# Kernel optimization log

Measured on AMD Instinct MI355X. Metric: run time of the kernel, lower is better.

## Reference

```python
import jax, jax.numpy as jnp
import numpy as np

B, S, H, DH = 1, 4096, 8, 40  # hardcoded in the original forward
D = H * DH  # 320

def setup_inputs() -> dict:
    key = jax.random.key(0)
    ks = jax.random.split(key, 6)
    s = 1.0 / np.sqrt(D)
    return {
        "x": jax.random.normal(ks[0], (B, S, D), dtype=jnp.float32),
        "Wq": jax.random.normal(ks[1], (D, D), dtype=jnp.float32) * s,
        "Wk": jax.random.normal(ks[2], (D, D), dtype=jnp.float32) * s,
        "Wv": jax.random.normal(ks[3], (D, D), dtype=jnp.float32) * s,
        "Wo": jax.random.normal(ks[4], (D, D), dtype=jnp.float32) * s,
        "bo": jnp.zeros((D,), dtype=jnp.float32),
    }

def reference(x, Wq, Wk, Wv, Wo, bo):
    scale = DH ** (-0.5)
    # nn.Linear(bias=False): y = x @ W^T. context = x (self-attention).
    q = x @ Wq.T
    k = x @ Wk.T
    v = x @ Wv.T
    # split heads: [B,S,D] -> [B*H, S, DH]
    def split_heads(t):
        return t.reshape(B, S, H, DH).transpose(0, 2, 1, 3).reshape(B * H, S, DH)
    q, k, v = split_heads(q), split_heads(k), split_heads(v)
    # fp32 QK^T (original forces float), softmax, AV
    sim = jnp.einsum('bid,bjd->bij', q.astype(jnp.float32), k.astype(jnp.float32)) * scale
    attn = jax.nn.softmax(sim, axis=-1)
    out = jnp.einsum('bij,bjd->bid', attn, v)
    # merge heads: [B*H, S, DH] -> [B, S, D]
    out = out.reshape(B, H, S, DH).transpose(0, 2, 1, 3).reshape(B, S, D)
    return out @ Wo.T + bo
```

## Files before the change

kernel.cpp:

```cpp
#include <hip/hip_runtime.h>
#include <math.h>


#define NS 4096
#define ND 320
#define SCALE2 0.2281101152f
#define HS48 196608
#define VTH 163840
#define XN 1310720

typedef __attribute__((ext_vector_type(8))) short bf16x8;
typedef __attribute__((ext_vector_type(16))) float f32x16;

static __device__ __forceinline__ unsigned short f2bru(float f) {
  return (unsigned short)((__builtin_bit_cast(unsigned int, f) + 0x8000u) >> 16);
}
static __device__ __forceinline__ unsigned int pk2ru(float a, float b) {
  unsigned int ua = __builtin_bit_cast(unsigned int, a) + 0x8000u;
  unsigned int ub = __builtin_bit_cast(unsigned int, b) + 0x8000u;
  return __builtin_amdgcn_perm(ub, ua, 0x07060302u);
}
static __device__ __forceinline__ unsigned int pk2t(float a, float b) {
  return __builtin_amdgcn_perm(__builtin_bit_cast(unsigned int, b),
                               __builtin_bit_cast(unsigned int, a), 0x07060302u);
}
static __device__ __forceinline__ float fexp2(float x) {
  return __builtin_amdgcn_exp2f(x);
}
static __device__ __forceinline__ bf16x8 ld8(const unsigned short* p) {
  union { uint2 u[2]; bf16x8 v; } c;
  c.u[0] = *(const uint2*)p;
  c.u[1] = *(const uint2*)(p + 4);
  return c.v;
}
static __device__ __forceinline__ uint4 ld16u(const unsigned short* p) {
  uint2 a = *(const uint2*)p, b = *(const uint2*)(p + 4);
  return make_uint4(a.x, a.y, b.x, b.y);
}
static __device__ __forceinline__ void st16(unsigned short* p, uint4 v) {
  *(uint2*)p = make_uint2(v.x, v.y);
  *(uint2*)(p + 4) = make_uint2(v.z, v.w);
}
static __device__ __forceinline__ int sig32(int q) {
  int s = q >> 4, h2 = (q >> 3) & 1, j = q & 7;
  return (s << 4) | ((j >> 2) << 3) | (h2 << 2) | (j & 3);
}

__global__ __launch_bounds__(256) void proj_qkv_kernel(
    const float* __restrict__ x, const float* __restrict__ Wq,
    const float* __restrict__ Wk, const float* __restrict__ Wv,
    unsigned short* __restrict__ Qp, unsigned short* __restrict__ Kp,
    unsigned short* __restrict__ Vt) {
  const int z = blockIdx.z;
  const float* W = (z == 0) ? Wq : (z == 1) ? Wk : Wv;
  __shared__ __align__(16) unsigned short As[64 * 36];
  __shared__ __align__(16) unsigned short Bs[64 * 36];
  __shared__ __align__(16) unsigned short Tile[64 * 76];
  const int t = threadIdx.x;
  const int w = t >> 6, l = t & 63, l31 = l & 31, hi = l >> 5;
  const int bm = blockIdx.x * 64, bn = blockIdx.y * 64;
  const int m0 = (w & 1) * 32, n0 = (w >> 1) * 32;
  f32x16 acc = {0,0,0,0,0,0,0,0,0,0,0,0,0,0,0,0};
  const int ar = t >> 2, ac = t & 3;
  const float* gA = x + (bm + ar) * ND + ac * 8;
  const float* gB = W + (bn + ar) * ND + ac * 8;
  unsigned short* lA = As + ar * 36 + ac * 8;
  unsigned short* lB = Bs + ar * 36 + ac * 8;
  const unsigned short* af = As + (m0 + l31) * 36 + hi * 8;
  const unsigned short* bf = Bs + (n0 + l31) * 36 + hi * 8;
  float4 a0 = *(const float4*)gA, a1 = *(const float4*)(gA + 4);
  float4 b0 = *(const float4*)gB, b1 = *(const float4*)(gB + 4);
  for (int k0 = 0; k0 < ND; k0 += 32) {
    __syncthreads();
    st16(lA, make_uint4(pk2ru(a0.x, a0.y), pk2ru(a0.z, a0.w),
                        pk2ru(a1.x, a1.y), pk2ru(a1.z, a1.w)));
    st16(lB, make_uint4(pk2ru(b0.x, b0.y), pk2ru(b0.z, b0.w),
                        pk2ru(b1.x, b1.y), pk2ru(b1.z, b1.w)));
    __syncthreads();
    if (k0 + 32 < ND) {
      gA += 32; gB += 32;
      a0 = *(const float4*)gA; a1 = *(const float4*)(gA + 4);
      b0 = *(const float4*)gB; b1 = *(const float4*)(gB + 4);
    }
    bf16x8 A0 = ld8(af), A1 = ld8(af + 16);
    bf16x8 B0 = ld8(bf), B1 = ld8(bf + 16);
    acc = __builtin_amdgcn_mfma_f32_32x32x16_bf16(A0, B0, acc, 0, 0, 0);
    acc = __builtin_amdgcn_mfma_f32_32x32x16_bf16(A1, B1, acc, 0, 0, 0);
  }
  if (z < 2) {
    unsigned short* Y = (z == 0) ? Qp : Kp;
    const float sc = (z == 0) ? SCALE2 : 1.0f;
    const unsigned int padw = (z == 0) ? 0xC200u : 0x3F80u;
#pragma unroll
    for (int r2 = 0; r2 < 16; r2++) {
      int lr = m0 + (r2 & 3) + 8 * (r2 >> 2) + 4 * hi;
      Tile[lr * 68 + n0 + l31] = f2bru(acc[r2] * sc);
    }
    __syncthreads();
    for (int i = t; i < 512; i += 256) {
      int row = i >> 3, ch = i & 7;
      int j = bn + ch * 8;
      int h = j / 40, dh = j - h * 40;
      uint4 v = ld16u(Tile + row * 68 + ch * 8);
      unsigned short* dst = Y + h * HS48 + (bm + row) * 48 + dh;
      st16(dst, v);
      if (dh == 0)
        st16(Y + h * HS48 + (bm + row) * 48 + 40, make_uint4(padw, 0u, 0u, 0u));
    }
  } else {
#pragma unroll
    for (int r2 = 0; r2 < 16; r2++) {
      int lr = m0 + (r2 & 3) + 8 * (r2 >> 2) + 4 * hi;
      Tile[(n0 + l31) * 76 + lr] = f2bru(acc[r2]);
    }
    __syncthreads();
    for (int i = t; i < 512; i += 256) {
      int row = i >> 3, ch = i & 7;
      int j = bn + row;
      int h = j / 40, dd = j - h * 40;
      uint4 v = ld16u(Tile + row * 76 + ch * 8);
      st16(Vt + h * VTH + dd * NS + bm + ch * 8, v);
    }
  }
}

__global__ __launch_bounds__(256) void attn_kernel(
    const unsigned short* __restrict__ Qp, const unsigned short* __restrict__ Kp,
    const unsigned short* __restrict__ Vt, unsigned short* __restrict__ Op,
    float* __restrict__ Lp) {
  const int b = blockIdx.x;
  const int h = b & 7, ks = (b >> 3) & 7, qt = b >> 6;
  const int t = threadIdx.x;
  const int w = t >> 6, l = t & 63, l31 = l & 31, hi = l >> 5;
  __shared__ __align__(16) unsigned short Ks[64 * 68];
  __shared__ __align__(16) unsigned short Vs[48 * 68];
  for (int i = t; i < 272; i += 256)
    ((unsigned int*)(Vs + 40 * 68))[i] = (i < 34) ? 0x3F803F80u : 0u;

  const int kbase = ks * 512;
  const int qbase = qt * 128 + w * 32;
  const unsigned short* qp = Qp + h * HS48 + (qbase + l31) * 48 + hi * 8;
  bf16x8 qf0 = *(const bf16x8*)qp;
  bf16x8 qf1 = *(const bf16x8*)(qp + 16);
  bf16x8 qf2 = *(const bf16x8*)(qp + 32);

  f32x16 oa0 = {0,0,0,0,0,0,0,0,0,0,0,0,0,0,0,0};
  f32x16 oa1 = {0,0,0,0,0,0,0,0,0,0,0,0,0,0,0,0};

  const int kr0 = t / 6, kc0 = t - kr0 * 6;
  const int kr1 = (t + 256) / 6, kc1 = (t + 256) - kr1 * 6;
  const unsigned short* gK0 = Kp + h * HS48 + (kbase + kr0) * 48 + kc0 * 8;
  const unsigned short* gK1 = Kp + h * HS48 + (kbase + kr1) * 48 + kc1 * 8;
  unsigned short* lK0 = Ks + ((kr0 & 32) | sig32(kr0 & 31)) * 68 + kc0 * 8;
  unsigned short* lK1 = Ks + ((kr1 & 32) | sig32(kr1 & 31)) * 68 + kc1 * 8;
  const int vr0 = t >> 3, vc = t & 7, vr1 = 32 + vr0;
  const unsigned short* gV0 = Vt + h * VTH + vr0 * NS + kbase + vc * 8;
  const unsigned short* gV1 = Vt + h * VTH + vr1 * NS + kbase + vc * 8;
  unsigned short* lV0 = Vs + vr0 * 68 + vc * 8;
  unsigned short* lV1 = Vs + vr1 * 68 + vc * 8;

  const unsigned short* kf0 = Ks + l31 * 68 + hi * 8;
  const unsigned short* kf1 = Ks + (32 + l31) * 68 + hi * 8;
  const unsigned short* vf0 = Vs + l31 * 68 + hi * 8;
  const unsigned short* vf1 = Vs + (32 + (l31 & 15)) * 68 + hi * 8;

  uint4 ka = *(const uint4*)gK0;
  uint4 kb2, vb2;
  uint4 va = *(const uint4*)gV0;
  if (t < 128) kb2 = *(const uint4*)gK1;
  if (t < 64)  vb2 = *(const uint4*)gV1;

  for (int it = 0; it < 8; ++it) {
    __syncthreads();
    st16(lK0, ka);
    if (t < 128) st16(lK1, kb2);
    st16(lV0, va);
    if (t < 64) st16(lV1, vb2);
    __syncthreads();
    gK0 += 64 * 48; gK1 += 64 * 48; gV0 += 64; gV1 += 64;
    ka = *(const uint4*)gK0;
    va = *(const uint4*)gV0;
    if (t < 128) kb2 = *(const uint4*)gK1;
    if (t < 64)  vb2 = *(const uint4*)gV1;

    unsigned int pw0[8], pw1[8];
    {
      f32x16 s0 = {0,0,0,0,0,0,0,0,0,0,0,0,0,0,0,0};
      s0 = __builtin_amdgcn_mfma_f32_32x32x16_bf16(ld8(kf0), qf0, s0, 0, 0, 0);
      s0 = __builtin_amdgcn_mfma_f32_32x32x16_bf16(ld8(kf0 + 16), qf1, s0, 0, 0, 0);
      s0 = __builtin_amdgcn_mfma_f32_32x32x16_bf16(ld8(kf0 + 32), qf2, s0, 0, 0, 0);
#pragma unroll
      for (int i = 0; i < 8; i++)
        pw0[i] = pk2t(fexp2(s0[2 * i]), fexp2(s0[2 * i + 1]));
    }
    {
      f32x16 s1 = {0,0,0,0,0,0,0,0,0,0,0,0,0,0,0,0};
      s1 = __builtin_amdgcn_mfma_f32_32x32x16_bf16(ld8(kf1), qf0, s1, 0, 0, 0);
      s1 = __builtin_amdgcn_mfma_f32_32x32x16_bf16(ld8(kf1 + 16), qf1, s1, 0, 0, 0);
      s1 = __builtin_amdgcn_mfma_f32_32x32x16_bf16(ld8(kf1 + 32), qf2, s1, 0, 0, 0);
#pragma unroll
      for (int i = 0; i < 8; i++)
        pw1[i] = pk2t(fexp2(s1[2 * i]), fexp2(s1[2 * i + 1]));
    }
    bf16x8 pf0 = __builtin_bit_cast(bf16x8, make_uint4(pw0[0], pw0[1], pw0[2], pw0[3]));
    bf16x8 pf1 = __builtin_bit_cast(bf16x8, make_uint4(pw0[4], pw0[5], pw0[6], pw0[7]));
    bf16x8 pf2 = __builtin_bit_cast(bf16x8, make_uint4(pw1[0], pw1[1], pw1[2], pw1[3]));
    bf16x8 pf3 = __builtin_bit_cast(bf16x8, make_uint4(pw1[4], pw1[5], pw1[6], pw1[7]));
    oa0 = __builtin_amdgcn_mfma_f32_32x32x16_bf16(pf0, ld8(vf0), oa0, 0, 0, 0);
    oa1 = __builtin_amdgcn_mfma_f32_32x32x16_bf16(pf0, ld8(vf1), oa1, 0, 0, 0);
    oa0 = __builtin_amdgcn_mfma_f32_32x32x16_bf16(pf1, ld8(vf0 + 16), oa0, 0, 0, 0);
    oa1 = __builtin_amdgcn_mfma_f32_32x32x16_bf16(pf1, ld8(vf1 + 16), oa1, 0, 0, 0);
    oa0 = __builtin_amdgcn_mfma_f32_32x32x16_bf16(pf2, ld8(vf0 + 32), oa0, 0, 0, 0);
    oa1 = __builtin_amdgcn_mfma_f32_32x32x16_bf16(pf2, ld8(vf1 + 32), oa1, 0, 0, 0);
    oa0 = __builtin_amdgcn_mfma_f32_32x32x16_bf16(pf3, ld8(vf0 + 48), oa0, 0, 0, 0);
    oa1 = __builtin_amdgcn_mfma_f32_32x32x16_bf16(pf3, ld8(vf1 + 48), oa1, 0, 0, 0);
  }

  unsigned short* opb = Op + ks * XN + h * 163840;
  float* lpb = Lp + ks * 32768 + h * NS;
#pragma unroll
  for (int r2 = 0; r2 < 16; r2++) {
    int qr = qbase + (r2 & 3) + 8 * (r2 >> 2) + 4 * hi;
    opb[qr * 40 + l31] = f2bru(oa0[r2]);
    if (l31 < 8) opb[qr * 40 + 32 + l31] = f2bru(oa1[r2]);
    if (l31 == 8) lpb[qr] = oa1[r2];
  }
}

__global__ __launch_bounds__(256) void proj_out_kernel(
    const unsigned short* __restrict__ Op, const float* __restrict__ Lp,
    const float* __restrict__ Wo, const float* __restrict__ bo,
    float* __restrict__ out) {
  __shared__ __align__(16) unsigned short As[64 * 36];
  __shared__ __align__(16) unsigned short Bs[64 * 36];
  __shared__ float invL[512];
  const int t = threadIdx.x;
  const int w = t >> 6, l = t & 63, l31 = l & 31, hi = l >> 5;
  const int bm = blockIdx.x * 64, bn = blockIdx.y * 64;
  const int m0 = (w & 1) * 32, n0 = (w >> 1) * 32;
  f32x16 acc = {0,0,0,0,0,0,0,0,0,0,0,0,0,0,0,0};
  const int ar = t >> 2, ac = t & 3;

  for (int i = t; i < 512; i += 256) {
    int h2 = i >> 6, sl = i & 63;
    float ls = 0.f;
#pragma unroll
    for (int k = 0; k < 8; k++) ls += Lp[k * 32768 + h2 * NS + bm + sl];
    invL[i] = 1.0f / ls;
  }

  const float* gB = Wo + (bn + ar) * ND + ac * 8;
  unsigned short* lA = As + ar * 36 + ac * 8;
  unsigned short* lB = Bs + ar * 36 + ac * 8;
  const unsigned short* af = As + (m0 + l31) * 36 + hi * 8;
  const unsigned short* bf = Bs + (n0 + l31) * 36 + hi * 8;

  int d0 = ac * 8;
  int h2 = d0 / 40, dh = d0 - h2 * 40;
  const unsigned short* opb = Op + h2 * 163840 + (bm + ar) * 40 + dh;
  uint4 u[8];
#pragma unroll
  for (int k = 0; k < 8; k++) u[k] = *(const uint4*)(opb + k * XN);
  float4 b0 = *(const float4*)gB, b1 = *(const float4*)(gB + 4);

  for (int k0 = 0; k0 < ND; k0 += 32) {
    __syncthreads();
    {
      float a0 = 0.f, a1 = 0.f, a2 = 0.f, a3 = 0.f;
      float a4 = 0.f, a5 = 0.f, a6 = 0.f, a7 = 0.f;
#pragma unroll
      for (int k = 0; k < 8; k++) {
        a0 += __builtin_bit_cast(float, u[k].x << 16);
        a1 += __builtin_bit_cast(float, u[k].x & 0xFFFF0000u);
        a2 += __builtin_bit_cast(float, u[k].y << 16);
        a3 += __builtin_bit_cast(float, u[k].y & 0xFFFF0000u);
        a4 += __builtin_bit_cast(float, u[k].z << 16);
        a5 += __builtin_bit_cast(float, u[k].z & 0xFFFF0000u);
        a6 += __builtin_bit_cast(float, u[k].w << 16);
        a7 += __builtin_bit_cast(float, u[k].w & 0xFFFF0000u);
      }
      float inv = invL[h2 * 64 + ar];
      st16(lA, make_uint4(pk2ru(a0 * inv, a1 * inv), pk2ru(a2 * inv, a3 * inv),
                          pk2ru(a4 * inv, a5 * inv), pk2ru(a6 * inv, a7 * inv)));
    }
    st16(lB, make_uint4(pk2ru(b0.x, b0.y), pk2ru(b0.z, b0.w),
                        pk2ru(b1.x, b1.y), pk2ru(b1.z, b1.w)));
    __syncthreads();
    if (k0 + 32 < ND) {
      d0 += 32;
      h2 = d0 / 40; dh = d0 - h2 * 40;
      opb = Op + h2 * 163840 + (bm + ar) * 40 + dh;
#pragma unroll
      for (int k = 0; k < 8; k++) u[k] = *(const uint4*)(opb + k * XN);
      gB += 32;
      b0 = *(const float4*)gB; b1 = *(const float4*)(gB + 4);
    }
    bf16x8 A0 = ld8(af), A1 = ld8(af + 16);
    bf16x8 B0 = ld8(bf), B1 = ld8(bf + 16);
    acc = __builtin_amdgcn_mfma_f32_32x32x16_bf16(A0, B0, acc, 0, 0, 0);
    acc = __builtin_amdgcn_mfma_f32_32x32x16_bf16(A1, B1, acc, 0, 0, 0);
  }
  const int j = bn + n0 + l31;
  const float bj = bo[j];
#pragma unroll
  for (int r2 = 0; r2 < 16; r2++) {
    int row = bm + m0 + (r2 & 3) + 8 * (r2 >> 2) + 4 * hi;
    out[row * ND + j] = acc[r2] + bj;
  }
}

extern "C" void kernel_launch(void* const* d_in, const int* in_sizes, int n_in,
                              void* d_out, int out_size, void* d_ws, size_t ws_size,
                              hipStream_t stream) {
  (void)in_sizes; (void)n_in; (void)out_size; (void)ws_size;
  const float* x  = (const float*)d_in[0];
  const float* Wq = (const float*)d_in[1];
  const float* Wk = (const float*)d_in[2];
  const float* Wv = (const float*)d_in[3];
  const float* Wo = (const float*)d_in[4];
  const float* bo = (const float*)d_in[5];
  float* out = (float*)d_out;

  unsigned short* Qp = (unsigned short*)d_ws;
  unsigned short* Kp = Qp + 8 * HS48;
  unsigned short* Vt = Kp + 8 * HS48;
  unsigned short* Op = Vt + 8 * VTH;
  float* Lp = (float*)(Op + 8 * XN);

  proj_qkv_kernel<<<dim3(64, 5, 3), 256, 0, stream>>>(x, Wq, Wk, Wv, Qp, Kp, Vt);
  attn_kernel<<<dim3(2048), 256, 0, stream>>>(Qp, Kp, Vt, Op, Lp);
  proj_out_kernel<<<dim3(64, 5), 256, 0, stream>>>(Op, Lp, Wo, bo, out);
}
```

Measured before the change: 135.4 us.

## Retile projections to 128x64 with K=64 and split combine into separate kernel

The QKV and output projection GEMMs move to 128x64 block tiles that step K by 64 and keep two accumulators per wave, which raises MFMA work per barrier and reuses each A fragment. The split-K attention partials are now reduced and normalized by a new combine kernel that writes a bf16 merged-head activation, so the output projection just loads it. The attention inner loop also interleaves the PV MFMAs with each score block to shorten live ranges. The cost is one extra kernel launch and an extra global round trip of the combined activation, and fewer blocks in the GEMMs, which lowers occupancy.

```diff
diff --git a/kernel.cpp b/kernel.cpp
--- a/kernel.cpp
+++ b/kernel.cpp
@@ -51,74 +51,91 @@
     const float* __restrict__ Wk, const float* __restrict__ Wv,
     unsigned short* __restrict__ Qp, unsigned short* __restrict__ Kp,
     unsigned short* __restrict__ Vt) {
-  const int z = blockIdx.z;
+  const int zi = blockIdx.y;
+  const int z = zi / 5;
+  const int bnn = (zi - z * 5) * 64;
   const float* W = (z == 0) ? Wq : (z == 1) ? Wk : Wv;
-  __shared__ __align__(16) unsigned short As[64 * 36];
-  __shared__ __align__(16) unsigned short Bs[64 * 36];
-  __shared__ __align__(16) unsigned short Tile[64 * 76];
+  __shared__ __align__(16) unsigned short As[128 * 76];
+  __shared__ __align__(16) unsigned short Bs[64 * 76];
   const int t = threadIdx.x;
   const int w = t >> 6, l = t & 63, l31 = l & 31, hi = l >> 5;
-  const int bm = blockIdx.x * 64, bn = blockIdx.y * 64;
-  const int m0 = (w & 1) * 32, n0 = (w >> 1) * 32;
-  f32x16 acc = {0,0,0,0,0,0,0,0,0,0,0,0,0,0,0,0};
-  const int ar = t >> 2, ac = t & 3;
-  const float* gA = x + (bm + ar) * ND + ac * 8;
-  const float* gB = W + (bn + ar) * ND + ac * 8;
-  unsigned short* lA = As + ar * 36 + ac * 8;
-  unsigned short* lB = Bs + ar * 36 + ac * 8;
-  const unsigned short* af = As + (m0 + l31) * 36 + hi * 8;
-  const unsigned short* bf = Bs + (n0 + l31) * 36 + hi * 8;
-  float4 a0 = *(const float4*)gA, a1 = *(const float4*)(gA + 4);
-  float4 b0 = *(const float4*)gB, b1 = *(const float4*)(gB + 4);
-  for (int k0 = 0; k0 < ND; k0 += 32) {
-    __syncthreads();
-    st16(lA, make_uint4(pk2ru(a0.x, a0.y), pk2ru(a0.z, a0.w),
-                        pk2ru(a1.x, a1.y), pk2ru(a1.z, a1.w)));
-    st16(lB, make_uint4(pk2ru(b0.x, b0.y), pk2ru(b0.z, b0.w),
-                        pk2ru(b1.x, b1.y), pk2ru(b1.z, b1.w)));
-    __syncthreads();
-    if (k0 + 32 < ND) {
-      gA += 32; gB += 32;
-      a0 = *(const float4*)gA; a1 = *(const float4*)(gA + 4);
-      b0 = *(const float4*)gB; b1 = *(const float4*)(gB + 4);
-    }
-    bf16x8 A0 = ld8(af), A1 = ld8(af + 16);
-    bf16x8 B0 = ld8(bf), B1 = ld8(bf + 16);
-    acc = __builtin_amdgcn_mfma_f32_32x32x16_bf16(A0, B0, acc, 0, 0, 0);
-    acc = __builtin_amdgcn_mfma_f32_32x32x16_bf16(A1, B1, acc, 0, 0, 0);
-  }
+  const int bm = blockIdx.x * 128;
+  const int m0 = w * 32;
+  f32x16 acc0 = {0,0,0,0,0,0,0,0,0,0,0,0,0,0,0,0};
+  f32x16 acc1 = {0,0,0,0,0,0,0,0,0,0,0,0,0,0,0,0};
+  const unsigned short* af = As + (m0 + l31) * 76 + hi * 8;
+  const unsigned short* bf0 = Bs + l31 * 76 + hi * 8;
+  const unsigned short* bf1 = Bs + (32 + l31) * 76 + hi * 8;
+  for (int k0 = 0; k0 < ND; k0 += 64) {
+    __syncthreads();
+#pragma unroll
+    for (int i = 0; i < 4; i++) {
+      int c = t + i * 256;
+      int row = c >> 3, kc = (c & 7) << 3;
+      const float* g = x + (bm + row) * ND + k0 + kc;
+      float4 v0 = *(const float4*)g, v1 = *(const float4*)(g + 4);
+      st16(As + row * 76 + kc,
+           make_uint4(pk2ru(v0.x, v0.y), pk2ru(v0.z, v0.w),
+                      pk2ru(v1.x, v1.y), pk2ru(v1.z, v1.w)));
+    }
+#pragma unroll
+    for (int i = 0; i < 2; i++) {
+      int c = t + i * 256;
+      int row = c >> 3, kc = (c & 7) << 3;
+      const float* g = W + (bnn + row) * ND + k0 + kc;
+      float4 v0 = *(const float4*)g, v1 = *(const float4*)(g + 4);
+      st16(Bs + row * 76 + kc,
+           make_uint4(pk2ru(v0.x, v0.y), pk2ru(v0.z, v0.w),
+                      pk2ru(v1.x, v1.y), pk2ru(v1.z, v1.w)));
+    }
+    __syncthreads();
+#pragma unroll
+    for (int ks = 0; ks < 4; ks++) {
+      bf16x8 A = ld8(af + ks * 16);
+      acc0 = __builtin_amdgcn_mfma_f32_32x32x16_bf16(A, ld8(bf0 + ks * 16), acc0, 0, 0, 0);
+      acc1 = __builtin_amdgcn_mfma_f32_32x32x16_bf16(A, ld8(bf1 + ks * 16), acc1, 0, 0, 0);
+    }
+  }
+  __syncthreads();
   if (z < 2) {
+    unsigned short* Tile = As;
     unsigned short* Y = (z == 0) ? Qp : Kp;
     const float sc = (z == 0) ? SCALE2 : 1.0f;
     const unsigned int padw = (z == 0) ? 0xC200u : 0x3F80u;
 #pragma unroll
     for (int r2 = 0; r2 < 16; r2++) {
       int lr = m0 + (r2 & 3) + 8 * (r2 >> 2) + 4 * hi;
-      Tile[lr * 68 + n0 + l31] = f2bru(acc[r2] * sc);
-    }
-    __syncthreads();
-    for (int i = t; i < 512; i += 256) {
-      int row = i >> 3, ch = i & 7;
-      int j = bn + ch * 8;
+      Tile[lr * 68 + l31] = f2bru(acc0[r2] * sc);
+      Tile[lr * 68 + 32 + l31] = f2bru(acc1[r2] * sc);
+    }
+    __syncthreads();
+#pragma unroll
+    for (int i = 0; i < 4; i++) {
+      int c = t + i * 256;
+      int row = c >> 3, ch = c & 7;
+      int j = bnn + ch * 8;
       int h = j / 40, dh = j - h * 40;
       uint4 v = ld16u(Tile + row * 68 + ch * 8);
-      unsigned short* dst = Y + h * HS48 + (bm + row) * 48 + dh;
-      st16(dst, v);
+      st16(Y + h * HS48 + (bm + row) * 48 + dh, v);
       if (dh == 0)
         st16(Y + h * HS48 + (bm + row) * 48 + 40, make_uint4(padw, 0u, 0u, 0u));
     }
   } else {
+    unsigned short* Tile = As;
 #pragma unroll
     for (int r2 = 0; r2 < 16; r2++) {
       int lr = m0 + (r2 & 3) + 8 * (r2 >> 2) + 4 * hi;
-      Tile[(n0 + l31) * 76 + lr] = f2bru(acc[r2]);
-    }
-    __syncthreads();
-    for (int i = t; i < 512; i += 256) {
-      int row = i >> 3, ch = i & 7;
-      int j = bn + row;
+      Tile[l31 * 132 + lr] = f2bru(acc0[r2]);
+      Tile[(32 + l31) * 132 + lr] = f2bru(acc1[r2]);
+    }
+    __syncthreads();
+#pragma unroll
+    for (int i = 0; i < 4; i++) {
+      int c = t + i * 256;
+      int row = c >> 4, ch = c & 15;
+      int j = bnn + row;
       int h = j / 40, dd = j - h * 40;
-      uint4 v = ld16u(Tile + row * 76 + ch * 8);
+      uint4 v = ld16u(Tile + row * 132 + ch * 8);
       st16(Vt + h * VTH + dd * NS + bm + ch * 8, v);
     }
   }
@@ -183,37 +200,38 @@
     if (t < 128) kb2 = *(const uint4*)gK1;
     if (t < 64)  vb2 = *(const uint4*)gV1;
 
-    unsigned int pw0[8], pw1[8];
     {
       f32x16 s0 = {0,0,0,0,0,0,0,0,0,0,0,0,0,0,0,0};
       s0 = __builtin_amdgcn_mfma_f32_32x32x16_bf16(ld8(kf0), qf0, s0, 0, 0, 0);
       s0 = __builtin_amdgcn_mfma_f32_32x32x16_bf16(ld8(kf0 + 16), qf1, s0, 0, 0, 0);
       s0 = __builtin_amdgcn_mfma_f32_32x32x16_bf16(ld8(kf0 + 32), qf2, s0, 0, 0, 0);
+      unsigned int pw[8];
 #pragma unroll
       for (int i = 0; i < 8; i++)
-        pw0[i] = pk2t(fexp2(s0[2 * i]), fexp2(s0[2 * i + 1]));
+        pw[i] = pk2t(fexp2(s0[2 * i]), fexp2(s0[2 * i + 1]));
+      bf16x8 pf0 = __builtin_bit_cast(bf16x8, make_uint4(pw[0], pw[1], pw[2], pw[3]));
+      bf16x8 pf1 = __builtin_bit_cast(bf16x8, make_uint4(pw[4], pw[5], pw[6], pw[7]));
+      oa0 = __builtin_amdgcn_mfma_f32_32x32x16_bf16(pf0, ld8(vf0), oa0, 0, 0, 0);
+      oa1 = __builtin_amdgcn_mfma_f32_32x32x16_bf16(pf0, ld8(vf1), oa1, 0, 0, 0);
+      oa0 = __builtin_amdgcn_mfma_f32_32x32x16_bf16(pf1, ld8(vf0 + 16), oa0, 0, 0, 0);
+      oa1 = __builtin_amdgcn_mfma_f32_32x32x16_bf16(pf1, ld8(vf1 + 16), oa1, 0, 0, 0);
     }
     {
       f32x16 s1 = {0,0,0,0,0,0,0,0,0,0,0,0,0,0,0,0};
       s1 = __builtin_amdgcn_mfma_f32_32x32x16_bf16(ld8(kf1), qf0, s1, 0, 0, 0);
       s1 = __builtin_amdgcn_mfma_f32_32x32x16_bf16(ld8(kf1 + 16), qf1, s1, 0, 0, 0);
       s1 = __builtin_amdgcn_mfma_f32_32x32x16_bf16(ld8(kf1 + 32), qf2, s1, 0, 0, 0);
+      unsigned int pw[8];
 #pragma unroll
       for (int i = 0; i < 8; i++)
-        pw1[i] = pk2t(fexp2(s1[2 * i]), fexp2(s1[2 * i + 1]));
-    }
-    bf16x8 pf0 = __builtin_bit_cast(bf16x8, make_uint4(pw0[0], pw0[1], pw0[2], pw0[3]));
-    bf16x8 pf1 = __builtin_bit_cast(bf16x8, make_uint4(pw0[4], pw0[5], pw0[6], pw0[7]));
-    bf16x8 pf2 = __builtin_bit_cast(bf16x8, make_uint4(pw1[0], pw1[1], pw1[2], pw1[3]));
-    bf16x8 pf3 = __builtin_bit_cast(bf16x8, make_uint4(pw1[4], pw1[5], pw1[6], pw1[7]));
-    oa0 = __builtin_amdgcn_mfma_f32_32x32x16_bf16(pf0, ld8(vf0), oa0, 0, 0, 0);
-    oa1 = __builtin_amdgcn_mfma_f32_32x32x16_bf16(pf0, ld8(vf1), oa1, 0, 0, 0);
-    oa0 = __builtin_amdgcn_mfma_f32_32x32x16_bf16(pf1, ld8(vf0 + 16), oa0, 0, 0, 0);
-    oa1 = __builtin_amdgcn_mfma_f32_32x32x16_bf16(pf1, ld8(vf1 + 16), oa1, 0, 0, 0);
-    oa0 = __builtin_amdgcn_mfma_f32_32x32x16_bf16(pf2, ld8(vf0 + 32), oa0, 0, 0, 0);
-    oa1 = __builtin_amdgcn_mfma_f32_32x32x16_bf16(pf2, ld8(vf1 + 32), oa1, 0, 0, 0);
-    oa0 = __builtin_amdgcn_mfma_f32_32x32x16_bf16(pf3, ld8(vf0 + 48), oa0, 0, 0, 0);
-    oa1 = __builtin_amdgcn_mfma_f32_32x32x16_bf16(pf3, ld8(vf1 + 48), oa1, 0, 0, 0);
+        pw[i] = pk2t(fexp2(s1[2 * i]), fexp2(s1[2 * i + 1]));
+      bf16x8 pf2 = __builtin_bit_cast(bf16x8, make_uint4(pw[0], pw[1], pw[2], pw[3]));
+      bf16x8 pf3 = __builtin_bit_cast(bf16x8, make_uint4(pw[4], pw[5], pw[6], pw[7]));
+      oa0 = __builtin_amdgcn_mfma_f32_32x32x16_bf16(pf2, ld8(vf0 + 32), oa0, 0, 0, 0);
+      oa1 = __builtin_amdgcn_mfma_f32_32x32x16_bf16(pf2, ld8(vf1 + 32), oa1, 0, 0, 0);
+      oa0 = __builtin_amdgcn_mfma_f32_32x32x16_bf16(pf3, ld8(vf0 + 48), oa0, 0, 0, 0);
+      oa1 = __builtin_amdgcn_mfma_f32_32x32x16_bf16(pf3, ld8(vf1 + 48), oa1, 0, 0, 0);
+    }
   }
 
   unsigned short* opb = Op + ks * XN + h * 163840;
@@ -227,85 +245,75 @@
   }
 }
 
+__global__ __launch_bounds__(256) void combine_kernel(
+    const unsigned short* __restrict__ Op, const float* __restrict__ Lp,
+    unsigned short* __restrict__ Xo) {
+  int e = (blockIdx.x * 256 + threadIdx.x) * 2;
+  int h = e / 163840;
+  int r = e - h * 163840;
+  int s = r / 40;
+  int dh = r - s * 40;
+  float a0 = 0.f, a1 = 0.f, lsum = 0.f;
+#pragma unroll
+  for (int k = 0; k < 8; k++) {
+    unsigned int u = *(const unsigned int*)(Op + k * XN + e);
+    a0 += __builtin_bit_cast(float, u << 16);
+    a1 += __builtin_bit_cast(float, u & 0xFFFF0000u);
+    lsum += Lp[k * 32768 + h * NS + s];
+  }
+  float inv = 1.0f / lsum;
+  *(unsigned int*)(Xo + s * ND + h * 40 + dh) = pk2ru(a0 * inv, a1 * inv);
+}
+
 __global__ __launch_bounds__(256) void proj_out_kernel(
-    const unsigned short* __restrict__ Op, const float* __restrict__ Lp,
-    const float* __restrict__ Wo, const float* __restrict__ bo,
-    float* __restrict__ out) {
-  __shared__ __align__(16) unsigned short As[64 * 36];
-  __shared__ __align__(16) unsigned short Bs[64 * 36];
-  __shared__ float invL[512];
+    const unsigned short* __restrict__ Xo, const float* __restrict__ Wo,
+    const float* __restrict__ bo, float* __restrict__ out) {
+  __shared__ __align__(16) unsigned short As[128 * 76];
+  __shared__ __align__(16) unsigned short Bs[64 * 76];
   const int t = threadIdx.x;
   const int w = t >> 6, l = t & 63, l31 = l & 31, hi = l >> 5;
-  const int bm = blockIdx.x * 64, bn = blockIdx.y * 64;
-  const int m0 = (w & 1) * 32, n0 = (w >> 1) * 32;
-  f32x16 acc = {0,0,0,0,0,0,0,0,0,0,0,0,0,0,0,0};
-  const int ar = t >> 2, ac = t & 3;
-
-  for (int i = t; i < 512; i += 256) {
-    int h2 = i >> 6, sl = i & 63;
-    float ls = 0.f;
-#pragma unroll
-    for (int k = 0; k < 8; k++) ls += Lp[k * 32768 + h2 * NS + bm + sl];
-    invL[i] = 1.0f / ls;
-  }
-
-  const float* gB = Wo + (bn + ar) * ND + ac * 8;
-  unsigned short* lA = As + ar * 36 + ac * 8;
-  unsigned short* lB = Bs + ar * 36 + ac * 8;
-  const unsigned short* af = As + (m0 + l31) * 36 + hi * 8;
-  const unsigned short* bf = Bs + (n0 + l31) * 36 + hi * 8;
-
-  int d0 = ac * 8;
-  int h2 = d0 / 40, dh = d0 - h2 * 40;
-  const unsigned short* opb = Op + h2 * 163840 + (bm + ar) * 40 + dh;
-  uint4 u[8];
-#pragma unroll
-  for (int k = 0; k < 8; k++) u[k] = *(const uint4*)(opb + k * XN);
-  float4 b0 = *(const float4*)gB, b1 = *(const float4*)(gB + 4);
-
-  for (int k0 = 0; k0 < ND; k0 += 32) {
-    __syncthreads();
-    {
-      float a0 = 0.f, a1 = 0.f, a2 = 0.f, a3 = 0.f;
-      float a4 = 0.f, a5 = 0.f, a6 = 0.f, a7 = 0.f;
-#pragma unroll
-      for (int k = 0; k < 8; k++) {
-        a0 += __builtin_bit_cast(float, u[k].x << 16);
-        a1 += __builtin_bit_cast(float, u[k].x & 0xFFFF0000u);
-        a2 += __builtin_bit_cast(float, u[k].y << 16);
-        a3 += __builtin_bit_cast(float, u[k].y & 0xFFFF0000u);
-        a4 += __builtin_bit_cast(float, u[k].z << 16);
-        a5 += __builtin_bit_cast(float, u[k].z & 0xFFFF0000u);
-        a6 += __builtin_bit_cast(float, u[k].w << 16);
-        a7 += __builtin_bit_cast(float, u[k].w & 0xFFFF0000u);
-      }
-      float inv = invL[h2 * 64 + ar];
-      st16(lA, make_uint4(pk2ru(a0 * inv, a1 * inv), pk2ru(a2 * inv, a3 * inv),
-                          pk2ru(a4 * inv, a5 * inv), pk2ru(a6 * inv, a7 * inv)));
-    }
-    st16(lB, make_uint4(pk2ru(b0.x, b0.y), pk2ru(b0.z, b0.w),
-                        pk2ru(b1.x, b1.y), pk2ru(b1.z, b1.w)));
-    __syncthreads();
-    if (k0 + 32 < ND) {
-      d0 += 32;
-      h2 = d0 / 40; dh = d0 - h2 * 40;
-      opb = Op + h2 * 163840 + (bm + ar) * 40 + dh;
-#pragma unroll
-      for (int k = 0; k < 8; k++) u[k] = *(const uint4*)(opb + k * XN);
-      gB += 32;
-      b0 = *(const float4*)gB; b1 = *(const float4*)(gB + 4);
-    }
-    bf16x8 A0 = ld8(af), A1 = ld8(af + 16);
-    bf16x8 B0 = ld8(bf), B1 = ld8(bf + 16);
-    acc = __builtin_amdgcn_mfma_f32_32x32x16_bf16(A0, B0, acc, 0, 0, 0);
-    acc = __builtin_amdgcn_mfma_f32_32x32x16_bf16(A1, B1, acc, 0, 0, 0);
-  }
-  const int j = bn + n0 + l31;
-  const float bj = bo[j];
+  const int bm = blockIdx.x * 128;
+  const int bnn = blockIdx.y * 64;
+  const int m0 = w * 32;
+  f32x16 acc0 = {0,0,0,0,0,0,0,0,0,0,0,0,0,0,0,0};
+  f32x16 acc1 = {0,0,0,0,0,0,0,0,0,0,0,0,0,0,0,0};
+  const unsigned short* af = As + (m0 + l31) * 76 + hi * 8;
+  const unsigned short* bf0 = Bs + l31 * 76 + hi * 8;
+  const unsigned short* bf1 = Bs + (32 + l31) * 76 + hi * 8;
+  for (int k0 = 0; k0 < ND; k0 += 64) {
+    __syncthreads();
+#pragma unroll
+    for (int i = 0; i < 4; i++) {
+      int c = t + i * 256;
+      int row = c >> 3, kc = (c & 7) << 3;
+      uint4 v = *(const uint4*)(Xo + (bm + row) * ND + k0 + kc);
+      st16(As + row * 76 + kc, v);
+    }
+#pragma unroll
+    for (int i = 0; i < 2; i++) {
+      int c = t + i * 256;
+      int row = c >> 3, kc = (c & 7) << 3;
+      const float* g = Wo + (bnn + row) * ND + k0 + kc;
+      float4 v0 = *(const float4*)g, v1 = *(const float4*)(g + 4);
+      st16(Bs + row * 76 + kc,
+           make_uint4(pk2ru(v0.x, v0.y), pk2ru(v0.z, v0.w),
+                      pk2ru(v1.x, v1.y), pk2ru(v1.z, v1.w)));
+    }
+    __syncthreads();
+#pragma unroll
+    for (int ks = 0; ks < 4; ks++) {
+      bf16x8 A = ld8(af + ks * 16);
+      acc0 = __builtin_amdgcn_mfma_f32_32x32x16_bf16(A, ld8(bf0 + ks * 16), acc0, 0, 0, 0);
+      acc1 = __builtin_amdgcn_mfma_f32_32x32x16_bf16(A, ld8(bf1 + ks * 16), acc1, 0, 0, 0);
+    }
+  }
+  const int j0 = bnn + l31, j1 = bnn + 32 + l31;
+  const float bj0 = bo[j0], bj1 = bo[j1];
 #pragma unroll
   for (int r2 = 0; r2 < 16; r2++) {
     int row = bm + m0 + (r2 & 3) + 8 * (r2 >> 2) + 4 * hi;
-    out[row * ND + j] = acc[r2] + bj;
+    out[row * ND + j0] = acc0[r2] + bj0;
+    out[row * ND + j1] = acc1[r2] + bj1;
   }
 }
 
@@ -324,10 +332,12 @@
   unsigned short* Qp = (unsigned short*)d_ws;
   unsigned short* Kp = Qp + 8 * HS48;
   unsigned short* Vt = Kp + 8 * HS48;
-  unsigned short* Op = Vt + 8 * VTH;
+  unsigned short* Xo = Vt + 8 * VTH;
+  unsigned short* Op = Xo + XN;
   float* Lp = (float*)(Op + 8 * XN);
 
-  proj_qkv_kernel<<<dim3(64, 5, 3), 256, 0, stream>>>(x, Wq, Wk, Wv, Qp, Kp, Vt);
+  proj_qkv_kernel<<<dim3(32, 15), 256, 0, stream>>>(x, Wq, Wk, Wv, Qp, Kp, Vt);
   attn_kernel<<<dim3(2048), 256, 0, stream>>>(Qp, Kp, Vt, Op, Lp);
-  proj_out_kernel<<<dim3(64, 5), 256, 0, stream>>>(Op, Lp, Wo, bo, out);
-}
+  combine_kernel<<<dim3(2560), 256, 0, stream>>>(Op, Lp, Xo);
+  proj_out_kernel<<<dim3(32, 5), 256, 0, stream>>>(Xo, Wo, bo, out);
+}
```

Measured after the change: 131.7 us. 1.03x faster.
